# Performance work log

Measured on AMD Instinct MI355X. Metric: run time of the kernel, lower is better.

Reference implementation:

```python
import jax, jax.numpy as jnp
import numpy as np

B, L, D, NH = 4, 1024, 1024, 16
DH = D // NH
H = 8 * D // 3  # SwiGLU hidden = 2730
NEG = -1e9


def setup_inputs() -> dict:
    key = jax.random.key(0)
    ks = jax.random.split(key, 8)
    init = lambda k, shape: (jax.random.normal(k, shape, jnp.float32) * 0.02)
    x = jax.random.normal(ks[0], (B, L, D), jnp.float32)
    causal = jnp.tril(jnp.ones((L, L), bool))
    m = jnp.where(causal, 0.0, NEG)[None, None].astype(jnp.float32)  # [1,1,L,L]
    return {
        'x': x,
        'm': m,
        'wx': init(ks[1], (D, 3 * D)),
        'bx': jnp.zeros((3 * D,), jnp.float32),
        'wo': init(ks[2], (D, D)),
        'bo': jnp.zeros((D,), jnp.float32),
        'mhanorm_w': jnp.ones((D,), jnp.float32),
        'ffnorm_w': jnp.ones((D,), jnp.float32),
        'u': init(ks[3], (D, H)),
        'v': init(ks[4], (D, H)),
        'w': init(ks[5], (H, D)),
    }


def rmsnorm(x, weight, eps=1e-8):
    rrms = jax.lax.rsqrt(jnp.mean(x * x, axis=-1, keepdims=True) + eps)
    return weight * x * rrms


def reference(x, m, wx, bx, wo, bo, mhanorm_w, ffnorm_w, u, v, w):
    scale = D ** (-0.5)  # note: original uses d**-0.5, NOT dh**-0.5
    qkv = rmsnorm(x, mhanorm_w) @ wx + bx                 # [B,L,3D]
    q, k, vv = jnp.split(qkv, 3, axis=-1)                  # each [B,L,D]
    split = lambda t: t.reshape(B, L, NH, DH).transpose(0, 2, 1, 3)  # [B,NH,L,DH]
    q, k, vv = split(q), split(k), split(vv)               # pe = identity (default)
    scores = jnp.einsum('bhic,bhjc->bhij', q, k) * scale + m
    A = jax.nn.softmax(scores, axis=-1)
    head = jnp.einsum('bhij,bhjc->bhic', A, vv)            # [B,NH,L,DH]
    head = head.transpose(0, 2, 1, 3).reshape(B, L, D)
    x = x + head @ wo + bo
    xn = rmsnorm(x, ffnorm_w)
    return x + (jax.nn.silu(xn @ u) * (xn @ v)) @ w
```

## Files before the change

### kernel.cpp

```cpp
#include <hip/hip_runtime.h>

#define B_  4
#define L_  1024
#define D_  1024
#define NH_ 16
#define DH_ 64
#define H_  2730
#define HP_ 2816
#define M_  4096

typedef short bf16x8 __attribute__((ext_vector_type(8)));
typedef float f32x4  __attribute__((ext_vector_type(4)));

__device__ __forceinline__ unsigned short f2bf(float f) {
    unsigned int u = __builtin_bit_cast(unsigned int, f);
    u += 0x7fffu + ((u >> 16) & 1u);
    return (unsigned short)(u >> 16);
}
__device__ __forceinline__ float bf2f(unsigned short s) {
    unsigned int u = ((unsigned int)s) << 16;
    return __builtin_bit_cast(float, u);
}

__device__ __forceinline__ void glds16(const void* g, void* l) {
    __builtin_amdgcn_global_load_lds(
        (const __attribute__((address_space(1))) unsigned int*)g,
        (__attribute__((address_space(3))) unsigned int*)l, 16, 0, 0);
}

__device__ __forceinline__ void xcd_swz(int& lx, int& ly) {
    const int gx = gridDim.x;
    const int flat = blockIdx.x + gx * blockIdx.y;
    const int r = flat & 7, q = flat >> 3;
    lx = q % gx;
    ly = r + 8 * (q / gx);
}

__global__ __launch_bounds__(256) void cvtT_kernel(
    const float* __restrict__ in, unsigned short* __restrict__ out,
    int K, int N, int Kp, int Np)
{
    __shared__ float t[32][33];
    const int k0 = blockIdx.x * 32, n0 = blockIdx.y * 32;
    const int tx = threadIdx.x & 31, ty = threadIdx.x >> 5;
    #pragma unroll
    for (int i = 0; i < 4; ++i) {
        const int k = k0 + ty + i * 8, n = n0 + tx;
        t[ty + i * 8][tx] = (k < K && n < N) ? in[(size_t)k * N + n] : 0.0f;
    }
    __syncthreads();
    #pragma unroll
    for (int i = 0; i < 4; ++i) {
        const int n = n0 + ty + i * 8, k = k0 + tx;
        out[(size_t)n * Kp + k] = f2bf(t[tx][ty + i * 8]);
    }
}

__global__ __launch_bounds__(256) void rmsnorm_kernel(
    const float* __restrict__ x, const float* __restrict__ w,
    unsigned short* __restrict__ out)
{
    const int row = blockIdx.x;
    const int t = threadIdx.x;
    const float4 v = ((const float4*)(x + (size_t)row * 1024))[t];
    float ss = v.x*v.x + v.y*v.y + v.z*v.z + v.w*v.w;
    #pragma unroll
    for (int off = 32; off > 0; off >>= 1) ss += __shfl_down(ss, off);
    __shared__ float red[4];
    if ((t & 63) == 0) red[t >> 6] = ss;
    __syncthreads();
    const float tot = red[0] + red[1] + red[2] + red[3];
    const float rr = rsqrtf(tot * (1.0f / 1024.0f) + 1e-8f);
    const float4 wv = ((const float4*)w)[t];
    ushort4 o;
    o.x = f2bf(v.x * wv.x * rr); o.y = f2bf(v.y * wv.y * rr);
    o.z = f2bf(v.z * wv.z * rr); o.w = f2bf(v.w * wv.w * rr);
    ((ushort4*)(out + (size_t)row * 1024))[t] = o;
}

template<int EPI, int TN>
__global__ __launch_bounds__(256) void gemm_bf16(
    const unsigned short* __restrict__ A, const unsigned short* __restrict__ Bt,
    int M, int N, int K,
    const float* __restrict__ bias, const float* __restrict__ res,
    float* __restrict__ outf, unsigned short* __restrict__ outb)
{
    constexpr int NS = TN / 32;
    constexpr int G  = (TN == 128) ? 4 : 3;
    constexpr int WAIT_G = 0xF70 | G;
    __shared__ __align__(16) unsigned short As[2][128 * 32];
    __shared__ __align__(16) unsigned short Bs[2][TN * 32];
    const int tid = threadIdx.x;
    int lx, ly;
    xcd_swz(lx, ly);
    const int m0 = ly * 128, n0 = lx * TN;
    const int lane = tid & 63, w = tid >> 6;
    const int wm = w >> 1, wn = w & 1;
    const int quad = lane >> 4, l15 = lane & 15;

    f32x4 acc[4][NS] = {};

    const int p0 = w * 64 + lane;
    const int r0 = p0 >> 2, c0 = (p0 & 3) ^ (r0 & 3);
    const int offL0 = p0 * 8, offL1 = 2048 + p0 * 8;

    const unsigned short* Ag0 = A + (size_t)(m0 + r0) * K + c0 * 8;
    const unsigned short* Ag1 = A + (size_t)(m0 + 64 + r0) * K + c0 * 8;
    const unsigned short* Bg0 = Bt + (size_t)(n0 + r0) * K + c0 * 8;
    const unsigned short* Bg1 = Bt + (size_t)(n0 + 64 + r0) * K + c0 * 8;

    auto stage = [&](int kk, int buf) {
        glds16(Ag0 + kk, &As[buf][offL0]);
        glds16(Ag1 + kk, &As[buf][offL1]);
        glds16(Bg0 + kk, &Bs[buf][offL0]);
        if (TN == 128) glds16(Bg1 + kk, &Bs[buf][offL1]);
    };
    auto compute = [&](int buf) {
        bf16x8 af[4], bfr[NS];
        #pragma unroll
        for (int ms = 0; ms < 4; ++ms) {
            const int row = wm * 64 + ms * 16 + l15;
            af[ms] = *(const bf16x8*)&As[buf][row * 32 + ((quad ^ (row & 3)) * 8)];
        }
        #pragma unroll
        for (int ns = 0; ns < NS; ++ns) {
            const int row = wn * (TN / 2) + ns * 16 + l15;
            bfr[ns] = *(const bf16x8*)&Bs[buf][row * 32 + ((quad ^ (row & 3)) * 8)];
        }
        #pragma unroll
        for (int ms = 0; ms < 4; ++ms)
            #pragma unroll
            for (int ns = 0; ns < NS; ++ns)
                acc[ms][ns] = __builtin_amdgcn_mfma_f32_16x16x32_bf16(
                    af[ms], bfr[ns], acc[ms][ns], 0, 0, 0);
    };

    const int nk = K >> 5;
    stage(0, 0);
    for (int i = 0; i < nk; i += 2) {
        if (i + 1 < nk) { stage((i + 1) << 5, 1); __builtin_amdgcn_s_waitcnt(WAIT_G); }
        else            { __builtin_amdgcn_s_waitcnt(0xF70); }
        __builtin_amdgcn_s_barrier();
        compute(0);
        __builtin_amdgcn_s_barrier();
        if (i + 2 < nk) { stage((i + 2) << 5, 0); __builtin_amdgcn_s_waitcnt(WAIT_G); }
        else            { __builtin_amdgcn_s_waitcnt(0xF70); }
        __builtin_amdgcn_s_barrier();
        compute(1);
        __builtin_amdgcn_s_barrier();
    }

    #pragma unroll
    for (int ms = 0; ms < 4; ++ms) {
        #pragma unroll
        for (int r = 0; r < 4; ++r) {
            const int row = m0 + wm * 64 + ms * 16 + quad * 4 + r;
            const size_t ro = (size_t)row * N;
            #pragma unroll
            for (int ns = 0; ns < NS; ++ns) {
                const int col = n0 + wn * (TN / 2) + ns * 16 + l15;
                float v = acc[ms][ns][r];
                if (EPI == 0) {
                    outb[ro + col] = f2bf(v + bias[col]);
                } else if (EPI == 1) {
                    outf[ro + col] = v + bias[col] + res[ro + col];
                } else {
                    outf[ro + col] = v + res[ro + col];
                }
            }
        }
    }
}

__global__ __launch_bounds__(256, 2) void gemm_swiglu(
    const unsigned short* __restrict__ A, const unsigned short* __restrict__ Bu,
    const unsigned short* __restrict__ Bv, unsigned short* __restrict__ g)
{
    constexpr int K = 1024, N = HP_;
    constexpr int WAIT_G = 0xF76;
    __shared__ __align__(16) unsigned short As[2][128 * 32];
    __shared__ __align__(16) unsigned short Us[2][128 * 32];
    __shared__ __align__(16) unsigned short Vs[2][128 * 32];
    const int tid = threadIdx.x;
    int lx, ly;
    xcd_swz(lx, ly);
    const int m0 = ly * 128, n0 = lx * 128;
    const int lane = tid & 63, w = tid >> 6;
    const int wm = w >> 1, wn = w & 1;
    const int quad = lane >> 4, l15 = lane & 15;

    f32x4 au[4][4] = {}, av[4][4] = {};

    const int p0 = w * 64 + lane;
    const int r0 = p0 >> 2, c0 = (p0 & 3) ^ (r0 & 3);
    const int offL0 = p0 * 8, offL1 = 2048 + p0 * 8;

    const unsigned short* Ag0 = A  + (size_t)(m0 + r0) * K + c0 * 8;
    const unsigned short* Ag1 = A  + (size_t)(m0 + 64 + r0) * K + c0 * 8;
    const unsigned short* Ug0 = Bu + (size_t)(n0 + r0) * K + c0 * 8;
    const unsigned short* Ug1 = Bu + (size_t)(n0 + 64 + r0) * K + c0 * 8;
    const unsigned short* Vg0 = Bv + (size_t)(n0 + r0) * K + c0 * 8;
    const unsigned short* Vg1 = Bv + (size_t)(n0 + 64 + r0) * K + c0 * 8;

    auto stage = [&](int kk, int buf) {
        glds16(Ag0 + kk, &As[buf][offL0]);
        glds16(Ag1 + kk, &As[buf][offL1]);
        glds16(Ug0 + kk, &Us[buf][offL0]);
        glds16(Ug1 + kk, &Us[buf][offL1]);
        glds16(Vg0 + kk, &Vs[buf][offL0]);
        glds16(Vg1 + kk, &Vs[buf][offL1]);
    };
    auto compute = [&](int buf) {
        bf16x8 af[4], uf[4], vf[4];
        #pragma unroll
        for (int ms = 0; ms < 4; ++ms) {
            const int row = wm * 64 + ms * 16 + l15;
            af[ms] = *(const bf16x8*)&As[buf][row * 32 + ((quad ^ (row & 3)) * 8)];
        }
        #pragma unroll
        for (int ns = 0; ns < 4; ++ns) {
            const int row = wn * 64 + ns * 16 + l15;
            uf[ns] = *(const bf16x8*)&Us[buf][row * 32 + ((quad ^ (row & 3)) * 8)];
            vf[ns] = *(const bf16x8*)&Vs[buf][row * 32 + ((quad ^ (row & 3)) * 8)];
        }
        #pragma unroll
        for (int ms = 0; ms < 4; ++ms)
            #pragma unroll
            for (int ns = 0; ns < 4; ++ns) {
                au[ms][ns] = __builtin_amdgcn_mfma_f32_16x16x32_bf16(af[ms], uf[ns], au[ms][ns], 0, 0, 0);
                av[ms][ns] = __builtin_amdgcn_mfma_f32_16x16x32_bf16(af[ms], vf[ns], av[ms][ns], 0, 0, 0);
            }
    };

    stage(0, 0);
    for (int i = 0; i < 32; i += 2) {
        if (i + 1 < 32) { stage((i + 1) << 5, 1); __builtin_amdgcn_s_waitcnt(WAIT_G); }
        else            { __builtin_amdgcn_s_waitcnt(0xF70); }
        __builtin_amdgcn_s_barrier();
        compute(0);
        __builtin_amdgcn_s_barrier();
        if (i + 2 < 32) { stage((i + 2) << 5, 0); __builtin_amdgcn_s_waitcnt(WAIT_G); }
        else            { __builtin_amdgcn_s_waitcnt(0xF70); }
        __builtin_amdgcn_s_barrier();
        compute(1);
        __builtin_amdgcn_s_barrier();
    }

    #pragma unroll
    for (int ms = 0; ms < 4; ++ms) {
        #pragma unroll
        for (int r = 0; r < 4; ++r) {
            const int row = m0 + wm * 64 + ms * 16 + quad * 4 + r;
            const size_t ro = (size_t)row * N;
            #pragma unroll
            for (int ns = 0; ns < 4; ++ns) {
                const int col = n0 + wn * 64 + ns * 16 + l15;
                const float uu = au[ms][ns][r];
                const float vv = av[ms][ns][r];
                g[ro + col] = f2bf(uu / (1.0f + __expf(-uu)) * vv);
            }
        }
    }
}

__global__ __launch_bounds__(256) void attn_mfma2_kernel(
    const unsigned short* __restrict__ qkv, unsigned short* __restrict__ hout)
{
    __shared__ __align__(16) unsigned short Qs[2][64 * 72];
    __shared__ __align__(16) unsigned short Ks[2][64 * 64];
    __shared__ __align__(16) unsigned short Vt[2][64 * 72];
    __shared__ __align__(16) unsigned short Ps[64 * 68];

    const int tid = threadIdx.x;
    const int qa = blockIdx.x, h = blockIdx.y, b = blockIdx.z;
    const int qb = 15 - qa;
    const int w = tid >> 6, lane = tid & 63;
    const int quad = lane >> 4, l15 = lane & 15;

    const size_t basek = (size_t)(b * L_) * 3072 + 1024 + h * 64;
    const size_t basev = basek + 1024;

    {
        const int row = tid >> 1, half = tid & 1;
        const int tile = row >> 6, r6 = row & 63;
        const int grow = (tile ? qb : qa) * 64 + r6;
        const unsigned short* gp = qkv + (size_t)(b * L_ + grow) * 3072 + h * 64 + half * 32;
        uint4 a = *(const uint4*)gp;
        uint4 c = *(const uint4*)(gp + 8);
        uint4 d = *(const uint4*)(gp + 16);
        uint4 e = *(const uint4*)(gp + 24);
        unsigned short* dp = &Qs[tile][r6 * 72 + half * 32];
        *(uint4*)dp = a; *(uint4*)(dp + 8) = c; *(uint4*)(dp + 16) = d; *(uint4*)(dp + 24) = e;
    }

    auto stageK = [&](int kt, int buf) {
        #pragma unroll
        for (int i = 0; i < 2; ++i) {
            const int p = i * 256 + tid;
            const int row = p >> 3;
            const int cc = (p & 7) ^ (row & 7);
            glds16(qkv + basek + (size_t)(kt * 64 + row) * 3072 + cc * 8, &Ks[buf][p * 8]);
        }
    };
    const int vkey = (tid & 31) * 2, vdp = tid >> 5;
    auto loadV = [&](int kt, uint4& v0, uint4& v1) {
        const unsigned short* gp = qkv + basev + (size_t)(kt * 64 + vkey) * 3072 + vdp * 8;
        v0 = *(const uint4*)gp;
        v1 = *(const uint4*)(gp + 3072);
    };
    auto writeV = [&](int buf, const uint4& v0, const uint4& v1) {
        union { uint4 u; unsigned short s[8]; } a, c;
        a.u = v0; c.u = v1;
        #pragma unroll
        for (int i = 0; i < 8; ++i) {
            unsigned int pk = (unsigned int)a.s[i] | ((unsigned int)c.s[i] << 16);
            *(unsigned int*)&Vt[buf][(vdp * 8 + i) * 72 + vkey] = pk;
        }
    };

    f32x4 O[4] = {};
    float m4[4], l4[4];
    #pragma unroll
    for (int r = 0; r < 4; ++r) { m4[r] = -1e30f; l4[r] = 0.0f; }

    stageK(0, 0);
    {
        uint4 v0, v1;
        loadV(0, v0, v1);
        writeV(0, v0, v1);
    }
    __syncthreads();

    bf16x8 af[2];
    #pragma unroll
    for (int s = 0; s < 2; ++s)
        af[s] = *(const bf16x8*)&Qs[0][(w * 16 + l15) * 72 + s * 32 + quad * 8];

    int qsel = 0, kt = 0;
    for (int t = 0; t < 17; ++t) {
        const int cb = t & 1, nb = cb ^ 1;
        const bool havenext = (t < 16);
        uint4 nv0, nv1;
        if (havenext) {
            const int ktn = (t + 1 <= qa) ? (t + 1) : (t - qa);
            stageK(ktn, nb);
            loadV(ktn, nv0, nv1);
        }

        bf16x8 bfk[4][2];
        #pragma unroll
        for (int n = 0; n < 4; ++n) {
            const int row = n * 16 + l15;
            #pragma unroll
            for (int s = 0; s < 2; ++s)
                bfk[n][s] = *(const bf16x8*)&Ks[cb][row * 64 + (((s * 4 + quad) ^ (row & 7)) * 8)];
        }
        f32x4 sacc[4] = {};
        #pragma unroll
        for (int n = 0; n < 4; ++n) {
            sacc[n] = __builtin_amdgcn_mfma_f32_16x16x32_bf16(af[0], bfk[n][0], sacc[n], 0, 0, 0);
            sacc[n] = __builtin_amdgcn_mfma_f32_16x16x32_bf16(af[1], bfk[n][1], sacc[n], 0, 0, 0);
        }

        const bool diag = (kt == (qsel ? qb : qa));
        float p[4][4], mx[4];
        #pragma unroll
        for (int r = 0; r < 4; ++r) mx[r] = -1e30f;
        #pragma unroll
        for (int n = 0; n < 4; ++n) {
            const int col = n * 16 + l15;
            #pragma unroll
            for (int r = 0; r < 4; ++r) {
                float v = sacc[n][r] * 0.03125f;
                if (diag && col > (w * 16 + quad * 4 + r)) v = -1e30f;
                p[n][r] = v;
                mx[r] = fmaxf(mx[r], v);
            }
        }
        #pragma unroll
        for (int r = 0; r < 4; ++r) {
            #pragma unroll
            for (int m = 1; m < 16; m <<= 1)
                mx[r] = fmaxf(mx[r], __shfl_xor(mx[r], m));
        }
        float alpha[4], rs[4];
        #pragma unroll
        for (int r = 0; r < 4; ++r) {
            const float mnew = fmaxf(m4[r], mx[r]);
            alpha[r] = __expf(m4[r] - mnew);
            m4[r] = mnew;
            float s0 = 0.0f;
            #pragma unroll
            for (int n = 0; n < 4; ++n) {
                const float e = __expf(p[n][r] - mnew);
                p[n][r] = e;
                s0 += e;
            }
            rs[r] = s0;
        }
        #pragma unroll
        for (int r = 0; r < 4; ++r) {
            #pragma unroll
            for (int m = 1; m < 16; m <<= 1)
                rs[r] += __shfl_xor(rs[r], m);
            l4[r] = l4[r] * alpha[r] + rs[r];
        }
        #pragma unroll
        for (int dn = 0; dn < 4; ++dn)
            #pragma unroll
            for (int r = 0; r < 4; ++r)
                O[dn][r] *= alpha[r];
        #pragma unroll
        for (int n = 0; n < 4; ++n)
            #pragma unroll
            for (int r = 0; r < 4; ++r)
                Ps[(w * 16 + quad * 4 + r) * 68 + n * 16 + l15] = f2bf(p[n][r]);

        if (havenext) writeV(nb, nv0, nv1);

        bf16x8 ap[2], bv[4][2];
        #pragma unroll
        for (int s = 0; s < 2; ++s)
            ap[s] = *(const bf16x8*)&Ps[(w * 16 + l15) * 68 + s * 32 + quad * 8];
        #pragma unroll
        for (int dn = 0; dn < 4; ++dn)
            #pragma unroll
            for (int s = 0; s < 2; ++s)
                bv[dn][s] = *(const bf16x8*)&Vt[cb][(dn * 16 + l15) * 72 + s * 32 + quad * 8];
        #pragma unroll
        for (int dn = 0; dn < 4; ++dn) {
            O[dn] = __builtin_amdgcn_mfma_f32_16x16x32_bf16(ap[0], bv[dn][0], O[dn], 0, 0, 0);
            O[dn] = __builtin_amdgcn_mfma_f32_16x16x32_bf16(ap[1], bv[dn][1], O[dn], 0, 0, 0);
        }

        if (t == qa) {
            #pragma unroll
            for (int r = 0; r < 4; ++r) {
                const float inv = 1.0f / l4[r];
                const int grow = qa * 64 + w * 16 + quad * 4 + r;
                unsigned short* op = hout + (size_t)(b * L_ + grow) * 1024 + h * 64;
                #pragma unroll
                for (int dn = 0; dn < 4; ++dn)
                    op[dn * 16 + l15] = f2bf(O[dn][r] * inv);
            }
            #pragma unroll
            for (int dn = 0; dn < 4; ++dn)
                #pragma unroll
                for (int r = 0; r < 4; ++r) O[dn][r] = 0.0f;
            #pragma unroll
            for (int r = 0; r < 4; ++r) { m4[r] = -1e30f; l4[r] = 0.0f; }
            qsel = 1;
            kt = 0;
            #pragma unroll
            for (int s = 0; s < 2; ++s)
                af[s] = *(const bf16x8*)&Qs[1][(w * 16 + l15) * 72 + s * 32 + quad * 8];
        } else {
            ++kt;
        }
        __syncthreads();
    }

    #pragma unroll
    for (int r = 0; r < 4; ++r) {
        const float inv = 1.0f / l4[r];
        const int grow = qb * 64 + w * 16 + quad * 4 + r;
        unsigned short* op = hout + (size_t)(b * L_ + grow) * 1024 + h * 64;
        #pragma unroll
        for (int dn = 0; dn < 4; ++dn)
            op[dn * 16 + l15] = f2bf(O[dn][r] * inv);
    }
}

extern "C" void kernel_launch(void* const* d_in, const int* in_sizes, int n_in,
                              void* d_out, int out_size, void* d_ws, size_t ws_size,
                              hipStream_t stream)
{
    const float* x   = (const float*)d_in[0];
    const float* wx  = (const float*)d_in[2];
    const float* bx  = (const float*)d_in[3];
    const float* wo  = (const float*)d_in[4];
    const float* bo  = (const float*)d_in[5];
    const float* mhw = (const float*)d_in[6];
    const float* ffw = (const float*)d_in[7];
    const float* u   = (const float*)d_in[8];
    const float* v   = (const float*)d_in[9];
    const float* w   = (const float*)d_in[10];
    float* out = (float*)d_out;

    char* W = (char*)d_ws;
    unsigned short* xn_bf   = (unsigned short*)(W + 0);
    unsigned short* wx_bf   = (unsigned short*)(W + 8388608);
    unsigned short* qkv_bf  = (unsigned short*)(W + 14680064);
    unsigned short* head_bf = (unsigned short*)(W + 39845888);
    unsigned short* wo_bf   = (unsigned short*)(W + 48234496);
    float*          x2      = (float*)(W + 50331648);
    unsigned short* u_bf    = (unsigned short*)(W + 67108864);
    unsigned short* v_bf    = (unsigned short*)(W + 72876032);
    unsigned short* w_bf    = (unsigned short*)(W + 78643200);
    unsigned short* g_bf    = (unsigned short*)(W + 84410368);

    cvtT_kernel<<<dim3(32, 96), 256, 0, stream>>>(wx, wx_bf, 1024, 3072, 1024, 3072);
    cvtT_kernel<<<dim3(32, 32), 256, 0, stream>>>(wo, wo_bf, 1024, 1024, 1024, 1024);
    cvtT_kernel<<<dim3(32, 88), 256, 0, stream>>>(u,  u_bf, 1024, 2730, 1024, 2816);
    cvtT_kernel<<<dim3(32, 88), 256, 0, stream>>>(v,  v_bf, 1024, 2730, 1024, 2816);
    cvtT_kernel<<<dim3(88, 32), 256, 0, stream>>>(w,  w_bf, 2730, 1024, 2816, 1024);

    rmsnorm_kernel<<<4096, 256, 0, stream>>>(x, mhw, xn_bf);

    gemm_bf16<0, 128><<<dim3(3072 / 128, 32), 256, 0, stream>>>(
        xn_bf, wx_bf, 4096, 3072, 1024, bx, nullptr, nullptr, qkv_bf);

    attn_mfma2_kernel<<<dim3(8, 16, 4), 256, 0, stream>>>(qkv_bf, head_bf);

    gemm_bf16<1, 64><<<dim3(1024 / 64, 32), 256, 0, stream>>>(
        head_bf, wo_bf, 4096, 1024, 1024, bo, x, x2, nullptr);

    rmsnorm_kernel<<<4096, 256, 0, stream>>>(x2, ffw, xn_bf);

    gemm_swiglu<<<dim3(2816 / 128, 32), 256, 0, stream>>>(xn_bf, u_bf, v_bf, g_bf);

    gemm_bf16<4, 64><<<dim3(1024 / 64, 32), 256, 0, stream>>>(
        g_bf, w_bf, 4096, 1024, 2816, nullptr, x2, out, nullptr);
}
```

Baseline: 360.1 us.

## Generalize GEMM pipelines to multi-stage LDS ring buffers and pad SwiGLU hidden dimension

Replaces the double-buffered K loop in both GEMM kernels with an S-stage LDS ring buffer: 3 stages for the QKV and SwiGLU GEMMs, 4 for the narrow-tile GEMMs. Each step issues a prefetch S-1 tiles ahead and waits with a matching vmcnt, so more global loads stay in flight. The SwiGLU hidden size is padded from 2816 to 3072, giving a 24-column grid with an explicit XCD-style block remap, and the g buffer now reuses the qkv workspace. This adds LDS per block, which can reduce occupancy, and the padding adds wasted MFMA work on zero columns.

```diff
diff --git a/kernel.cpp b/kernel.cpp
--- a/kernel.cpp
+++ b/kernel.cpp
@@ -6,7 +6,7 @@
 #define NH_ 16
 #define DH_ 64
 #define H_  2730
-#define HP_ 2816
+#define HP3 3072
 #define M_  4096
 
 typedef short bf16x8 __attribute__((ext_vector_type(8)));
@@ -78,7 +78,7 @@
     ((ushort4*)(out + (size_t)row * 1024))[t] = o;
 }
 
-template<int EPI, int TN>
+template<int EPI, int TN, int S>
 __global__ __launch_bounds__(256) void gemm_bf16(
     const unsigned short* __restrict__ A, const unsigned short* __restrict__ Bt,
     int M, int N, int K,
@@ -87,9 +87,9 @@
 {
     constexpr int NS = TN / 32;
     constexpr int G  = (TN == 128) ? 4 : 3;
-    constexpr int WAIT_G = 0xF70 | G;
-    __shared__ __align__(16) unsigned short As[2][128 * 32];
-    __shared__ __align__(16) unsigned short Bs[2][TN * 32];
+    constexpr int WAIT = 0xF70 | ((S - 1) * G);
+    __shared__ __align__(16) unsigned short As[S][128 * 32];
+    __shared__ __align__(16) unsigned short Bs[S][TN * 32];
     const int tid = threadIdx.x;
     int lx, ly;
     xcd_swz(lx, ly);
@@ -136,17 +136,20 @@
     };
 
     const int nk = K >> 5;
-    stage(0, 0);
-    for (int i = 0; i < nk; i += 2) {
-        if (i + 1 < nk) { stage((i + 1) << 5, 1); __builtin_amdgcn_s_waitcnt(WAIT_G); }
-        else            { __builtin_amdgcn_s_waitcnt(0xF70); }
+    #pragma unroll
+    for (int s = 0; s < S - 1; ++s) stage(s << 5, s);
+    int cb = 0, sb = S - 1;
+    for (int i = 0; i < nk; ++i) {
+        if (i + S - 1 < nk) {
+            stage((i + S - 1) << 5, sb);
+            sb = (sb + 1 == S) ? 0 : sb + 1;
+            __builtin_amdgcn_s_waitcnt(WAIT);
+        } else {
+            __builtin_amdgcn_s_waitcnt(0xF70);
+        }
         __builtin_amdgcn_s_barrier();
-        compute(0);
-        __builtin_amdgcn_s_barrier();
-        if (i + 2 < nk) { stage((i + 2) << 5, 0); __builtin_amdgcn_s_waitcnt(WAIT_G); }
-        else            { __builtin_amdgcn_s_waitcnt(0xF70); }
-        __builtin_amdgcn_s_barrier();
-        compute(1);
+        compute(cb);
+        cb = (cb + 1 == S) ? 0 : cb + 1;
         __builtin_amdgcn_s_barrier();
     }
 
@@ -176,14 +179,16 @@
     const unsigned short* __restrict__ A, const unsigned short* __restrict__ Bu,
     const unsigned short* __restrict__ Bv, unsigned short* __restrict__ g)
 {
-    constexpr int K = 1024, N = HP_;
-    constexpr int WAIT_G = 0xF76;
-    __shared__ __align__(16) unsigned short As[2][128 * 32];
-    __shared__ __align__(16) unsigned short Us[2][128 * 32];
-    __shared__ __align__(16) unsigned short Vs[2][128 * 32];
+    constexpr int K = 1024, N = HP3, S = 3;
+    constexpr int WAIT = 0xF70 | 12;
+    __shared__ __align__(16) unsigned short As[S][128 * 32];
+    __shared__ __align__(16) unsigned short Us[S][128 * 32];
+    __shared__ __align__(16) unsigned short Vs[S][128 * 32];
     const int tid = threadIdx.x;
-    int lx, ly;
-    xcd_swz(lx, ly);
+    const int flat = blockIdx.x + 24 * blockIdx.y;
+    const int rr = flat & 7, q = flat >> 3;
+    const int lx = rr + 8 * (q % 3);
+    const int ly = q / 3;
     const int m0 = ly * 128, n0 = lx * 128;
     const int lane = tid & 63, w = tid >> 6;
     const int wm = w >> 1, wn = w & 1;
@@ -232,17 +237,21 @@
             }
     };
 
-    stage(0, 0);
-    for (int i = 0; i < 32; i += 2) {
-        if (i + 1 < 32) { stage((i + 1) << 5, 1); __builtin_amdgcn_s_waitcnt(WAIT_G); }
-        else            { __builtin_amdgcn_s_waitcnt(0xF70); }
+    constexpr int nk = K >> 5;
+    #pragma unroll
+    for (int s = 0; s < S - 1; ++s) stage(s << 5, s);
+    int cb = 0, sb = S - 1;
+    for (int i = 0; i < nk; ++i) {
+        if (i + S - 1 < nk) {
+            stage((i + S - 1) << 5, sb);
+            sb = (sb + 1 == S) ? 0 : sb + 1;
+            __builtin_amdgcn_s_waitcnt(WAIT);
+        } else {
+            __builtin_amdgcn_s_waitcnt(0xF70);
+        }
         __builtin_amdgcn_s_barrier();
-        compute(0);
-        __builtin_amdgcn_s_barrier();
-        if (i + 2 < 32) { stage((i + 2) << 5, 0); __builtin_amdgcn_s_waitcnt(WAIT_G); }
-        else            { __builtin_amdgcn_s_waitcnt(0xF70); }
-        __builtin_amdgcn_s_barrier();
-        compute(1);
+        compute(cb);
+        cb = (cb + 1 == S) ? 0 : cb + 1;
         __builtin_amdgcn_s_barrier();
     }
 
@@ -495,30 +504,30 @@
     unsigned short* wo_bf   = (unsigned short*)(W + 48234496);
     float*          x2      = (float*)(W + 50331648);
     unsigned short* u_bf    = (unsigned short*)(W + 67108864);
-    unsigned short* v_bf    = (unsigned short*)(W + 72876032);
-    unsigned short* w_bf    = (unsigned short*)(W + 78643200);
-    unsigned short* g_bf    = (unsigned short*)(W + 84410368);
+    unsigned short* v_bf    = (unsigned short*)(W + 73400320);
+    unsigned short* w_bf    = (unsigned short*)(W + 79691776);
+    unsigned short* g_bf    = qkv_bf;
 
     cvtT_kernel<<<dim3(32, 96), 256, 0, stream>>>(wx, wx_bf, 1024, 3072, 1024, 3072);
     cvtT_kernel<<<dim3(32, 32), 256, 0, stream>>>(wo, wo_bf, 1024, 1024, 1024, 1024);
-    cvtT_kernel<<<dim3(32, 88), 256, 0, stream>>>(u,  u_bf, 1024, 2730, 1024, 2816);
-    cvtT_kernel<<<dim3(32, 88), 256, 0, stream>>>(v,  v_bf, 1024, 2730, 1024, 2816);
-    cvtT_kernel<<<dim3(88, 32), 256, 0, stream>>>(w,  w_bf, 2730, 1024, 2816, 1024);
+    cvtT_kernel<<<dim3(32, 96), 256, 0, stream>>>(u,  u_bf, 1024, 2730, 1024, 3072);
+    cvtT_kernel<<<dim3(32, 96), 256, 0, stream>>>(v,  v_bf, 1024, 2730, 1024, 3072);
+    cvtT_kernel<<<dim3(96, 32), 256, 0, stream>>>(w,  w_bf, 2730, 1024, 3072, 1024);
 
     rmsnorm_kernel<<<4096, 256, 0, stream>>>(x, mhw, xn_bf);
 
-    gemm_bf16<0, 128><<<dim3(3072 / 128, 32), 256, 0, stream>>>(
+    gemm_bf16<0, 128, 3><<<dim3(24, 32), 256, 0, stream>>>(
         xn_bf, wx_bf, 4096, 3072, 1024, bx, nullptr, nullptr, qkv_bf);
 
     attn_mfma2_kernel<<<dim3(8, 16, 4), 256, 0, stream>>>(qkv_bf, head_bf);
 
-    gemm_bf16<1, 64><<<dim3(1024 / 64, 32), 256, 0, stream>>>(
+    gemm_bf16<1, 64, 4><<<dim3(16, 32), 256, 0, stream>>>(
         head_bf, wo_bf, 4096, 1024, 1024, bo, x, x2, nullptr);
 
     rmsnorm_kernel<<<4096, 256, 0, stream>>>(x2, ffw, xn_bf);
 
-    gemm_swiglu<<<dim3(2816 / 128, 32), 256, 0, stream>>>(xn_bf, u_bf, v_bf, g_bf);
-
-    gemm_bf16<4, 64><<<dim3(1024 / 64, 32), 256, 0, stream>>>(
-        g_bf, w_bf, 4096, 1024, 2816, nullptr, x2, out, nullptr);
-}
+    gemm_swiglu<<<dim3(24, 32), 256, 0, stream>>>(xn_bf, u_bf, v_bf, g_bf);
+
+    gemm_bf16<4, 64, 4><<<dim3(16, 32), 256, 0, stream>>>(
+        g_bf, w_bf, 4096, 1024, 3072, nullptr, x2, out, nullptr);
+}
```

New measurement: 365.1 us. No clear change (+1.4%).
